# Kernel optimization log

Hardware: AMD Instinct MI355X
Metric: run time of the kernel (lower is better)

Reference implementation:

```python
import jax, jax.numpy as jnp
import numpy as np

EPS = 1e-5  # BatchNorm eps (torch default)

def _bn(x, gamma, beta):
    # training-mode BatchNorm over the edge/node (leading) axis, biased var
    mean = x.mean(axis=0, keepdims=True)
    var = x.var(axis=0, keepdims=True)
    return (x - mean) * jax.lax.rsqrt(var + EPS) * gamma + beta

def _silu(x):
    return x * jax.nn.sigmoid(x)

def setup_inputs() -> dict:
    N, E, H, NH = 50000, 800000, 128, 4
    HD = H // NH
    key = jax.random.key(0)
    ks = jax.random.split(key, 8)
    x = jax.random.normal(ks[0], (N, H), dtype=jnp.float32)
    weight = jax.random.uniform(ks[1], (N, 1), dtype=jnp.float32)  # positive fraction weights
    src = jax.random.randint(ks[2], (E,), 0, N)
    dst = jax.random.randint(ks[3], (E,), 0, N)
    # f: Linear(2H, 1) + BN(1)
    Wf = jax.random.normal(ks[4], (2 * H, 1), dtype=jnp.float32) * 0.05
    bf = jnp.zeros((1,), jnp.float32)
    f_gamma = jnp.ones((1,), jnp.float32)
    f_beta = jnp.zeros((1,), jnp.float32)
    # g: NH heads of Linear(2H, HD) + BN(HD), stacked on leading head axis
    Wg = jax.random.normal(ks[5], (NH, 2 * H, HD), dtype=jnp.float32) * 0.05
    bg = jnp.zeros((NH, HD), jnp.float32)
    g_gamma = jnp.ones((NH, HD), jnp.float32)
    g_beta = jnp.zeros((NH, HD), jnp.float32)
    # bn_nodes: BN(H)
    n_gamma = jnp.ones((H,), jnp.float32)
    n_beta = jnp.zeros((H,), jnp.float32)
    return dict(x=x, weight=weight, src=src, dst=dst, Wf=Wf, bf=bf,
                f_gamma=f_gamma, f_beta=f_beta, Wg=Wg, bg=bg,
                g_gamma=g_gamma, g_beta=g_beta, n_gamma=n_gamma, n_beta=n_beta)

def reference(x, weight, src, dst, Wf, bf, f_gamma, f_beta, Wg, bg, g_gamma, g_beta, n_gamma, n_beta):
    N = x.shape[0]
    E = src.shape[0]
    # per-edge concat of src/dst node features: [E, 2H]
    hihj = jnp.concatenate([x[src], x[dst]], axis=-1)
    # attention logit f(hihj) = SiLU(BN(Linear)) then exp: [E, 1]
    exp_e = jnp.exp(_silu(_bn(hihj @ Wf + bf, f_gamma, f_beta)))
    # weighted softmax-like normalization over incoming edges of each dst node
    we = weight[src] * exp_e                                   # [E, 1]
    sum_w_exp = jax.ops.segment_sum(we, dst, num_segments=N)   # [N, 1]
    a = we / sum_w_exp[dst]                                    # [E, 1]
    # multi-head message: a_ij * SiLU(BN(Linear_h(hihj))) per head, concat
    z = jnp.einsum('ed,hdk->ehk', hihj, Wg) + bg               # [E, NH, HD]
    z = _silu(_bn(z, g_gamma, g_beta))
    msg = (a[:, :, None] * z).reshape(E, -1)                   # [E, H]
    h = jax.ops.segment_sum(msg, dst, num_segments=N)          # [N, H]
    out = _bn(h, n_gamma, n_beta) + x                          # residual
    return out
```

## Files before the change

kernel.cpp:

```cpp
#include <hip/hip_runtime.h>
#include <hip/hip_bf16.h>
#include <math.h>

#define HDIM 128
#define PAD 64
typedef unsigned short ushort_t;
typedef unsigned int uint_t;
typedef __attribute__((ext_vector_type(8))) short bf16x8;
typedef __attribute__((ext_vector_type(4))) float f32x4;
typedef __attribute__((ext_vector_type(2))) float v2f;

__device__ __forceinline__ float wave_allreduce(float v){
  #pragma unroll
  for (int o = 1; o < 64; o <<= 1) v += __shfl_xor(v, o);
  return v;
}

__device__ __forceinline__ ushort_t f2bf(float f){
  uint_t u = __float_as_uint(f);
  uint_t r = (u + 0x7fffu + ((u >> 16) & 1u)) >> 16;
  return (ushort_t)r;
}

__device__ __forceinline__ v2f bf2(uint_t u){
  v2f r;
  r.x = __uint_as_float(u << 16);
  r.y = __uint_as_float(u & 0xffff0000u);
  return r;
}

__global__ __launch_bounds__(128) void k_wpack(const float* __restrict__ Wg,
    const float* __restrict__ Wf, ushort_t* __restrict__ W2t,
    int* __restrict__ cnt, int N){
  int b = blockIdx.x;
  int k = threadIdx.x;
  if (b < 272){
    float val;
    if (b < 128)       val = Wg[(size_t)(b >> 5) * 8192 + k * 32 + (b & 31)];
    else if (b < 256){ int c2 = b - 128;
                       val = Wg[(size_t)(c2 >> 5) * 8192 + (k + 128) * 32 + (c2 & 31)]; }
    else if (b == 256) val = Wf[k];
    else if (b == 257) val = Wf[128 + k];
    else               val = 0.f;
    W2t[(size_t)b * 128 + k] = f2bf(val);
  } else {
    int i = (b - 272) * 128 + k;
    if (i < N) cnt[i] = 0;
  }
}

__global__ __launch_bounds__(256) void k_gemmfill(const float* __restrict__ x,
    const ushort_t* __restrict__ W2t, const float* __restrict__ weight,
    ushort_t* __restrict__ Pb, ushort_t* __restrict__ Qb,
    float* __restrict__ v, float2* __restrict__ uw2,
    const int* __restrict__ src, const int* __restrict__ dst,
    int* __restrict__ cnt, int* __restrict__ es,
    int N, int E, int GB){
  if ((int)blockIdx.x < GB){
    int wid = __builtin_amdgcn_readfirstlane(threadIdx.x >> 6);
    int lane = threadIdx.x & 63;
    int quad = lane >> 4, col = lane & 15;
    int strip = blockIdx.x * 2 + (wid >> 1);
    int half = wid & 1;
    int n_base = strip * 16;
    if (n_base >= N) return;
    int tbeg = half * 8;
    int ntile = half ? 9 : 8;
    f32x4 acc[9];
    #pragma unroll
    for (int t = 0; t < 9; ++t) acc[t] = (f32x4){0.f, 0.f, 0.f, 0.f};
    int row = n_base + col;
    int rowc = row < N ? row : N - 1;
    const float* xr = x + (size_t)rowc * HDIM + quad * 8;
    #pragma unroll
    for (int kk = 0; kk < 4; ++kk){
      float4 a0 = *(const float4*)(xr + kk * 32);
      float4 a1 = *(const float4*)(xr + kk * 32 + 4);
      bf16x8 af;
      af[0] = (short)f2bf(a0.x); af[1] = (short)f2bf(a0.y);
      af[2] = (short)f2bf(a0.z); af[3] = (short)f2bf(a0.w);
      af[4] = (short)f2bf(a1.x); af[5] = (short)f2bf(a1.y);
      af[6] = (short)f2bf(a1.z); af[7] = (short)f2bf(a1.w);
      const ushort_t* wb = W2t + (size_t)(tbeg * 16) * 128 + (size_t)col * 128 + kk * 32 + quad * 8;
      #pragma unroll
      for (int t = 0; t < 9; ++t){
        if (t < ntile){
          bf16x8 bfr = *(const bf16x8*)(wb + (size_t)t * 16 * 128);
          acc[t] = __builtin_amdgcn_mfma_f32_16x16x32_bf16(af, bfr, acc[t], 0, 0, 0);
        }
      }
    }
    #pragma unroll
    for (int t = 0; t < 8; ++t){
      int ct = tbeg + t;
      int c = ct * 16 + col;
      #pragma unroll
      for (int r = 0; r < 4; ++r){
        int n = n_base + quad * 4 + r;
        if (n < N){
          ushort_t valb = f2bf(acc[t][r]);
          if (c < 128) Pb[(size_t)n * HDIM + c] = valb;
          else         Qb[(size_t)n * HDIM + (c - 128)] = valb;
        }
      }
    }
    if (half){
      #pragma unroll
      for (int r = 0; r < 4; ++r){
        int n = n_base + quad * 4 + r;
        if (n < N){
          float val = acc[8][r];
          if (col == 0)      uw2[n] = make_float2(val, weight[n]);
          else if (col == 1) v[n] = val;
        }
      }
    }
  } else {
    int bi = blockIdx.x - GB;
    int part = bi & 7;
    int nch = (gridDim.x - GB) >> 3;
    int chunk = bi >> 3;
    int Npp = (N + 7) >> 3;
    int lo = part * Npp;
    int hi = lo + Npp; if (hi > N) hi = N;
    int stride = nch * 256;
    int e = chunk * 256 + threadIdx.x;
#define FILL1(d, s) if ((d) >= lo && (d) < hi){ \
      int c = atomicAdd(&cnt[d], 1); \
      if (c < PAD) es[(size_t)(d) * PAD + c] = (s); }
    for (; e + 7 * stride < E; e += 8 * stride){
      int d0 = dst[e],            d1 = dst[e + stride];
      int d2 = dst[e + 2*stride], d3 = dst[e + 3*stride];
      int d4 = dst[e + 4*stride], d5 = dst[e + 5*stride];
      int d6 = dst[e + 6*stride], d7 = dst[e + 7*stride];
      int s0 = src[e],            s1 = src[e + stride];
      int s2 = src[e + 2*stride], s3 = src[e + 3*stride];
      int s4 = src[e + 4*stride], s5 = src[e + 5*stride];
      int s6 = src[e + 6*stride], s7 = src[e + 7*stride];
      FILL1(d0, s0) FILL1(d1, s1) FILL1(d2, s2) FILL1(d3, s3)
      FILL1(d4, s4) FILL1(d5, s5) FILL1(d6, s6) FILL1(d7, s7)
    }
    for (; e < E; e += stride){
      int d = dst[e];
      FILL1(d, src[e])
    }
#undef FILL1
  }
}

__global__ __launch_bounds__(256) void k_gstats(const ushort_t* __restrict__ Pb,
    const ushort_t* __restrict__ Qb, const float* __restrict__ v,
    const float2* __restrict__ uw2, const int* __restrict__ es,
    const int* __restrict__ cnt, float* __restrict__ pstatG, int N, int GB){
  int lane = threadIdx.x & 63;
  int wid = __builtin_amdgcn_readfirstlane(threadIdx.x >> 6);
  int part = ((int)blockIdx.x - GB) & 7;
  int Npp = (N + 7) >> 3;
  int lo = part * Npp;
  int hi = lo + Npp; if (hi > N) hi = N;
  int step = (gridDim.x >> 3) << 2;
  const uint_t* Pu = (const uint_t*)Pb;
  const uint_t* Qu = (const uint_t*)Qb;
  v2f gs = {0.f, 0.f}, gq = {0.f, 0.f};
  float fs = 0.f, fq = 0.f;
  int n = lo + ((blockIdx.x >> 3) << 2) + wid;
  int dnA = 0, sjA = 0; uint_t qA = 0; float vA = 0.f;
  if (n < hi){
    dnA = cnt[n];
    sjA = es[(size_t)n * PAD + lane];
    qA  = Qu[(size_t)n * 64 + lane];
    vA  = v[n];
  }
  while (n < hi){
    int nn = n + step;
    int dnB = 0, sjB = 0; uint_t qB = 0; float vB = 0.f;
    if (nn < hi){
      dnB = cnt[nn];
      sjB = es[(size_t)nn * PAD + lane];
      qB  = Qu[(size_t)nn * 64 + lane];
      vB  = v[nn];
    }
    int dn = dnA < PAD ? dnA : PAD;
    int sj = sjA;
    if (lane < dn){
      float2 uw = uw2[sj];
      float t = uw.x + vA;
      fs += t; fq = fmaf(t, t, fq);
    }
    v2f q = bf2(qA);
    int j = 0;
#define GSTAT(p) { v2f y = bf2(p) + q; gs += y; \
                   gq.x = fmaf(y.x, y.x, gq.x); gq.y = fmaf(y.y, y.y, gq.y); }
    for (; j + 7 < dn; j += 8){
      int s0=__shfl(sj,j),   s1=__shfl(sj,j+1), s2=__shfl(sj,j+2), s3=__shfl(sj,j+3);
      int s4=__shfl(sj,j+4), s5=__shfl(sj,j+5), s6=__shfl(sj,j+6), s7=__shfl(sj,j+7);
      uint_t p0=Pu[(size_t)s0*64+lane], p1=Pu[(size_t)s1*64+lane];
      uint_t p2=Pu[(size_t)s2*64+lane], p3=Pu[(size_t)s3*64+lane];
      uint_t p4=Pu[(size_t)s4*64+lane], p5=Pu[(size_t)s5*64+lane];
      uint_t p6=Pu[(size_t)s6*64+lane], p7=Pu[(size_t)s7*64+lane];
      GSTAT(p0) GSTAT(p1) GSTAT(p2) GSTAT(p3)
      GSTAT(p4) GSTAT(p5) GSTAT(p6) GSTAT(p7)
    }
    for (; j + 3 < dn; j += 4){
      int s0=__shfl(sj,j), s1=__shfl(sj,j+1), s2=__shfl(sj,j+2), s3=__shfl(sj,j+3);
      uint_t p0=Pu[(size_t)s0*64+lane], p1=Pu[(size_t)s1*64+lane];
      uint_t p2=Pu[(size_t)s2*64+lane], p3=Pu[(size_t)s3*64+lane];
      GSTAT(p0) GSTAT(p1) GSTAT(p2) GSTAT(p3)
    }
    for (; j < dn; ++j){
      int s0 = __shfl(sj, j);
      uint_t p0 = Pu[(size_t)s0*64+lane];
      GSTAT(p0)
    }
#undef GSTAT
    n = nn; dnA = dnB; sjA = sjB; qA = qB; vA = vB;
  }
  fs = wave_allreduce(fs); fq = wave_allreduce(fq);
  __shared__ float red[4][258];
  red[wid][2*lane]       = gs.x; red[wid][2*lane+1]   = gs.y;
  red[wid][128+2*lane]   = gq.x; red[wid][129+2*lane] = gq.y;
  if (lane == 0){ red[wid][256] = fs; red[wid][257] = fq; }
  __syncthreads();
  for (int c = threadIdx.x; c < 258; c += 256)
    pstatG[(size_t)blockIdx.x * 258 + c] = red[0][c] + red[1][c] + red[2][c] + red[3][c];
}

__global__ __launch_bounds__(256) void k_redfin1(const float* __restrict__ pstatG,
    int NB, const float* __restrict__ g_gamma, const float* __restrict__ g_beta,
    const float* __restrict__ f_gamma, const float* __restrict__ f_beta,
    float* __restrict__ fin, long long E){
  int j = blockIdx.x;
  int c1 = (j < 128) ? j : 256;
  int c2 = (j < 128) ? 128 + j : 257;
  double s1 = 0, s2 = 0;
  for (int b = threadIdx.x; b < NB; b += 256){
    const float* pb = pstatG + (size_t)b * 258;
    s1 += (double)pb[c1]; s2 += (double)pb[c2];
  }
  __shared__ double m1[256], m2[256];
  m1[threadIdx.x] = s1; m2[threadIdx.x] = s2;
  __syncthreads();
  for (int o = 128; o; o >>= 1){
    if (threadIdx.x < o){ m1[threadIdx.x] += m1[threadIdx.x + o];
                          m2[threadIdx.x] += m2[threadIdx.x + o]; }
    __syncthreads();
  }
  if (threadIdx.x == 0){
    double m = m1[0] / (double)E;
    double var = m2[0] / (double)E - m * m;
    if (j < 128){
      float sc = (float)((double)g_gamma[j] / sqrt(var + 1e-5));
      fin[2 + j] = sc; fin[130 + j] = g_beta[j] - (float)m * sc;
    } else {
      float sc = (float)((double)f_gamma[0] / sqrt(var + 1e-5));
      fin[0] = sc; fin[1] = f_beta[0] - (float)m * sc;
    }
  }
}

__global__ __launch_bounds__(256) void k_msg(const ushort_t* __restrict__ Pb,
    const ushort_t* __restrict__ Qb, const float* __restrict__ v,
    const float2* __restrict__ uw2, const int* __restrict__ es,
    const int* __restrict__ cnt, const float* __restrict__ fin,
    float* __restrict__ h, float* __restrict__ pstatH, int N, int GB){
  int lane = threadIdx.x & 63;
  int wid = __builtin_amdgcn_readfirstlane(threadIdx.x >> 6);
  int part = ((int)blockIdx.x - GB) & 7;
  int Npp = (N + 7) >> 3;
  int lo = part * Npp;
  int hi = lo + Npp; if (hi > N) hi = N;
  int step = (gridDim.x >> 3) << 2;
  const uint_t* Pu = (const uint_t*)Pb;
  const uint_t* Qu = (const uint_t*)Qb;
  float fsc = fin[0], fsh = fin[1];
  v2f gsc = {fin[2 + 2*lane], fin[3 + 2*lane]};
  v2f gsh = {fin[130 + 2*lane], fin[131 + 2*lane]};
  v2f hs = {0.f, 0.f}, hq = {0.f, 0.f};
  int n = lo + ((blockIdx.x >> 3) << 2) + wid;
  int dnA = 0, sjA = 0; uint_t qA = 0; float vA = 0.f;
  if (n < hi){
    dnA = cnt[n];
    sjA = es[(size_t)n * PAD + lane];
    qA  = Qu[(size_t)n * 64 + lane];
    vA  = v[n];
  }
  while (n < hi){
    int nn = n + step;
    int dnB = 0, sjB = 0; uint_t qB = 0; float vB = 0.f;
    if (nn < hi){
      dnB = cnt[nn];
      sjB = es[(size_t)nn * PAD + lane];
      qB  = Qu[(size_t)nn * 64 + lane];
      vB  = v[nn];
    }
    int dn = dnA < PAD ? dnA : PAD;
    int sj = sjA;
    float wj = 0.f;
    if (lane < dn){
      float2 uw = uw2[sj];
      float tt = fmaf(uw.x + vA, fsc, fsh);
      float sl = tt * __builtin_amdgcn_rcpf(1.f + __expf(-tt));
      wj = uw.y * __expf(sl);
    }
    v2f q = bf2(qA);
    v2f acc = {0.f, 0.f};
    int j = 0;
#define EDGE(p,a) { v2f y = (bf2(p) + q) * gsc + gsh; \
      float e0 = __expf(-y.x), e1 = __expf(-y.y); \
      float d0 = 1.f + e0, d1 = 1.f + e1; \
      float r = __builtin_amdgcn_rcpf(d0 * d1) * a; \
      acc.x = fmaf(y.x * d1, r, acc.x); acc.y = fmaf(y.y * d0, r, acc.y); }
    for (; j + 7 < dn; j += 8){
      int s0=__shfl(sj,j),   s1=__shfl(sj,j+1), s2=__shfl(sj,j+2), s3=__shfl(sj,j+3);
      int s4=__shfl(sj,j+4), s5=__shfl(sj,j+5), s6=__shfl(sj,j+6), s7=__shfl(sj,j+7);
      float a0=__shfl(wj,j),   a1=__shfl(wj,j+1), a2=__shfl(wj,j+2), a3=__shfl(wj,j+3);
      float a4=__shfl(wj,j+4), a5=__shfl(wj,j+5), a6=__shfl(wj,j+6), a7=__shfl(wj,j+7);
      uint_t p0=Pu[(size_t)s0*64+lane], p1=Pu[(size_t)s1*64+lane];
      uint_t p2=Pu[(size_t)s2*64+lane], p3=Pu[(size_t)s3*64+lane];
      uint_t p4=Pu[(size_t)s4*64+lane], p5=Pu[(size_t)s5*64+lane];
      uint_t p6=Pu[(size_t)s6*64+lane], p7=Pu[(size_t)s7*64+lane];
      EDGE(p0,a0) EDGE(p1,a1) EDGE(p2,a2) EDGE(p3,a3)
      EDGE(p4,a4) EDGE(p5,a5) EDGE(p6,a6) EDGE(p7,a7)
    }
    for (; j + 3 < dn; j += 4){
      int s0=__shfl(sj,j), s1=__shfl(sj,j+1), s2=__shfl(sj,j+2), s3=__shfl(sj,j+3);
      float a0=__shfl(wj,j), a1=__shfl(wj,j+1), a2=__shfl(wj,j+2), a3=__shfl(wj,j+3);
      uint_t p0=Pu[(size_t)s0*64+lane], p1=Pu[(size_t)s1*64+lane];
      uint_t p2=Pu[(size_t)s2*64+lane], p3=Pu[(size_t)s3*64+lane];
      EDGE(p0,a0) EDGE(p1,a1) EDGE(p2,a2) EDGE(p3,a3)
    }
    for (; j < dn; ++j){
      int s0 = __shfl(sj, j);
      float a0 = __shfl(wj, j);
      uint_t p0 = Pu[(size_t)s0*64+lane];
      EDGE(p0,a0)
    }
#undef EDGE
    float sw = wave_allreduce(wj);
    float rs = (dn > 0) ? (1.f / sw) : 0.f;
    acc.x *= rs; acc.y *= rs;
    *(float2*)&h[(size_t)n * 128 + 2*lane] = make_float2(acc.x, acc.y);
    hs += acc; hq += acc * acc;
    n = nn; dnA = dnB; sjA = sjB; qA = qB; vA = vB;
  }
  __shared__ float red[4][256];
  red[wid][2*lane]       = hs.x; red[wid][2*lane+1]   = hs.y;
  red[wid][128+2*lane]   = hq.x; red[wid][129+2*lane] = hq.y;
  __syncthreads();
  int c = threadIdx.x;
  pstatH[(size_t)blockIdx.x * 256 + c] = red[0][c] + red[1][c] + red[2][c] + red[3][c];
}

__global__ __launch_bounds__(256) void k_redfin2(const float* __restrict__ pstatH,
    int NB, const float* __restrict__ n_gamma, const float* __restrict__ n_beta,
    float* __restrict__ fin, int N){
  int j = blockIdx.x;
  double s1 = 0, s2 = 0;
  for (int b = threadIdx.x; b < NB; b += 256){
    const float* pb = pstatH + (size_t)b * 256;
    s1 += (double)pb[j]; s2 += (double)pb[128 + j];
  }
  __shared__ double m1[256], m2[256];
  m1[threadIdx.x] = s1; m2[threadIdx.x] = s2;
  __syncthreads();
  for (int o = 128; o; o >>= 1){
    if (threadIdx.x < o){ m1[threadIdx.x] += m1[threadIdx.x + o];
                          m2[threadIdx.x] += m2[threadIdx.x + o]; }
    __syncthreads();
  }
  if (threadIdx.x == 0){
    double m = m1[0] / (double)N;
    double var = m2[0] / (double)N - m * m;
    float sc = (float)((double)n_gamma[j] / sqrt(var + 1e-5));
    fin[258 + j] = sc; fin[386 + j] = n_beta[j] - (float)m * sc;
  }
}

__global__ __launch_bounds__(256) void k_out(const float* __restrict__ h,
    const float* __restrict__ x, const float* __restrict__ fin,
    float* __restrict__ out, int total4){
  int i = blockIdx.x * 256 + threadIdx.x;
  if (i >= total4) return;
  const float4* h4 = (const float4*)h; const float4* x4 = (const float4*)x;
  float4 hv = h4[i], xv = x4[i];
  int c = (i * 4) & 127;
  float4 o;
  o.x = fmaf(hv.x, fin[258 + c],     fin[386 + c])     + xv.x;
  o.y = fmaf(hv.y, fin[258 + c + 1], fin[386 + c + 1]) + xv.y;
  o.z = fmaf(hv.z, fin[258 + c + 2], fin[386 + c + 2]) + xv.z;
  o.w = fmaf(hv.w, fin[258 + c + 3], fin[386 + c + 3]) + xv.w;
  ((float4*)out)[i] = o;
}

extern "C" void kernel_launch(void* const* d_in, const int* in_sizes, int n_in,
                              void* d_out, int out_size, void* d_ws, size_t ws_size,
                              hipStream_t stream){
  const float* x       = (const float*)d_in[0];
  const float* weight  = (const float*)d_in[1];
  const int*   src     = (const int*)d_in[2];
  const int*   dst     = (const int*)d_in[3];
  const float* Wf      = (const float*)d_in[4];
  const float* f_gamma = (const float*)d_in[6];
  const float* f_beta  = (const float*)d_in[7];
  const float* Wg      = (const float*)d_in[8];
  const float* g_gamma = (const float*)d_in[10];
  const float* g_beta  = (const float*)d_in[11];
  const float* n_gamma = (const float*)d_in[12];
  const float* n_beta  = (const float*)d_in[13];
  float* out = (float*)d_out;

  int N = in_sizes[0] / HDIM;
  int E = in_sizes[2];

  char* ws = (char*)d_ws;
  size_t off = 0;
  auto alloc = [&](size_t bytes)->char*{
    char* p = ws + off; off = (off + bytes + 255) & ~(size_t)255; return p;
  };
  ushort_t* Pb    = (ushort_t*)alloc((size_t)N * HDIM * 2);
  ushort_t* Qb    = (ushort_t*)alloc((size_t)N * HDIM * 2);
  float* h        = (float*)alloc((size_t)N * HDIM * 4);
  float* v        = (float*)alloc((size_t)N * 4);
  float2* uw2     = (float2*)alloc((size_t)N * 8);
  int* es         = (int*)alloc((size_t)N * PAD * 4);
  ushort_t* W2t   = (ushort_t*)alloc((size_t)272 * 128 * 2);
  int* cnt        = (int*)alloc((size_t)N * 4);
  const int NWB = 2048;
  const int NB  = NWB;
  float*  pstatG = (float*)alloc((size_t)NB * 258 * 4);
  float*  pstatH = (float*)alloc((size_t)NB * 256 * 4);
  float*  fin    = (float*)alloc(514 * 4);

  int GB = (N + 31) / 32;
  const int FB = 1024;

  k_wpack   <<<272 + (N + 127) / 128, 128, 0, stream>>>(Wg, Wf, W2t, cnt, N);
  k_gemmfill<<<GB + FB, 256, 0, stream>>>(x, W2t, weight, Pb, Qb, v, uw2,
                                          src, dst, cnt, es, N, E, GB);
  k_gstats  <<<NWB, 256, 0, stream>>>(Pb, Qb, v, uw2, es, cnt, pstatG, N, GB);
  k_redfin1 <<<129, 256, 0, stream>>>(pstatG, NB, g_gamma, g_beta, f_gamma, f_beta, fin, (long long)E);
  k_msg     <<<NWB, 256, 0, stream>>>(Pb, Qb, v, uw2, es, cnt, fin, h, pstatH, N, GB);
  k_redfin2 <<<128, 256, 0, stream>>>(pstatH, NB, n_gamma, n_beta, fin, N);
  k_out     <<<(N * HDIM / 4 + 255) / 256, 256, 0, stream>>>(h, x, fin, out, N * HDIM / 4);
}
```

Baseline: 272.9 us.

## Split fused gemm/fill kernel and pad per-node atomic counters to avoid contention

Splits the combined GEMM+edge-bucketing kernel into separate k_fill and k_gemm launches, doubles fill blocks, and zeroes counters with hipMemsetAsync. Per-node counters are strided by 16 ints (64 bytes) so atomics on neighbouring nodes hit different cache lines, reducing false sharing. The cost is a larger, sparser counter array (more memset traffic and scattered reads in the stats and message kernels), and the fill and GEMM work no longer overlap within one launch.

```diff
diff --git a/kernel.cpp b/kernel.cpp
--- a/kernel.cpp
+++ b/kernel.cpp
@@ -4,6 +4,7 @@
 
 #define HDIM 128
 #define PAD 64
+#define CSTR 16
 typedef unsigned short ushort_t;
 typedef unsigned int uint_t;
 typedef __attribute__((ext_vector_type(8))) short bf16x8;
@@ -30,131 +31,123 @@
 }
 
 __global__ __launch_bounds__(128) void k_wpack(const float* __restrict__ Wg,
-    const float* __restrict__ Wf, ushort_t* __restrict__ W2t,
-    int* __restrict__ cnt, int N){
+    const float* __restrict__ Wf, ushort_t* __restrict__ W2t){
   int b = blockIdx.x;
   int k = threadIdx.x;
-  if (b < 272){
-    float val;
-    if (b < 128)       val = Wg[(size_t)(b >> 5) * 8192 + k * 32 + (b & 31)];
-    else if (b < 256){ int c2 = b - 128;
-                       val = Wg[(size_t)(c2 >> 5) * 8192 + (k + 128) * 32 + (c2 & 31)]; }
-    else if (b == 256) val = Wf[k];
-    else if (b == 257) val = Wf[128 + k];
-    else               val = 0.f;
-    W2t[(size_t)b * 128 + k] = f2bf(val);
-  } else {
-    int i = (b - 272) * 128 + k;
-    if (i < N) cnt[i] = 0;
-  }
-}
-
-__global__ __launch_bounds__(256) void k_gemmfill(const float* __restrict__ x,
+  float val;
+  if (b < 128)       val = Wg[(size_t)(b >> 5) * 8192 + k * 32 + (b & 31)];
+  else if (b < 256){ int c2 = b - 128;
+                     val = Wg[(size_t)(c2 >> 5) * 8192 + (k + 128) * 32 + (c2 & 31)]; }
+  else if (b == 256) val = Wf[k];
+  else if (b == 257) val = Wf[128 + k];
+  else               val = 0.f;
+  W2t[(size_t)b * 128 + k] = f2bf(val);
+}
+
+__global__ __launch_bounds__(256) void k_gemm(const float* __restrict__ x,
     const ushort_t* __restrict__ W2t, const float* __restrict__ weight,
     ushort_t* __restrict__ Pb, ushort_t* __restrict__ Qb,
-    float* __restrict__ v, float2* __restrict__ uw2,
+    float* __restrict__ v, float2* __restrict__ uw2, int N){
+  int wid = __builtin_amdgcn_readfirstlane(threadIdx.x >> 6);
+  int lane = threadIdx.x & 63;
+  int quad = lane >> 4, col = lane & 15;
+  int strip = blockIdx.x * 2 + (wid >> 1);
+  int half = wid & 1;
+  int n_base = strip * 16;
+  if (n_base >= N) return;
+  int tbeg = half * 8;
+  int ntile = half ? 9 : 8;
+  f32x4 acc[9];
+  #pragma unroll
+  for (int t = 0; t < 9; ++t) acc[t] = (f32x4){0.f, 0.f, 0.f, 0.f};
+  int row = n_base + col;
+  int rowc = row < N ? row : N - 1;
+  const float* xr = x + (size_t)rowc * HDIM + quad * 8;
+  #pragma unroll
+  for (int kk = 0; kk < 4; ++kk){
+    float4 a0 = *(const float4*)(xr + kk * 32);
+    float4 a1 = *(const float4*)(xr + kk * 32 + 4);
+    bf16x8 af;
+    af[0] = (short)f2bf(a0.x); af[1] = (short)f2bf(a0.y);
+    af[2] = (short)f2bf(a0.z); af[3] = (short)f2bf(a0.w);
+    af[4] = (short)f2bf(a1.x); af[5] = (short)f2bf(a1.y);
+    af[6] = (short)f2bf(a1.z); af[7] = (short)f2bf(a1.w);
+    const ushort_t* wb = W2t + (size_t)(tbeg * 16) * 128 + (size_t)col * 128 + kk * 32 + quad * 8;
+    #pragma unroll
+    for (int t = 0; t < 9; ++t){
+      if (t < ntile){
+        bf16x8 bfr = *(const bf16x8*)(wb + (size_t)t * 16 * 128);
+        acc[t] = __builtin_amdgcn_mfma_f32_16x16x32_bf16(af, bfr, acc[t], 0, 0, 0);
+      }
+    }
+  }
+  #pragma unroll
+  for (int t = 0; t < 8; ++t){
+    int ct = tbeg + t;
+    int c = ct * 16 + col;
+    #pragma unroll
+    for (int r = 0; r < 4; ++r){
+      int n = n_base + quad * 4 + r;
+      if (n < N){
+        ushort_t valb = f2bf(acc[t][r]);
+        if (c < 128) Pb[(size_t)n * HDIM + c] = valb;
+        else         Qb[(size_t)n * HDIM + (c - 128)] = valb;
+      }
+    }
+  }
+  if (half){
+    #pragma unroll
+    for (int r = 0; r < 4; ++r){
+      int n = n_base + quad * 4 + r;
+      if (n < N){
+        float val = acc[8][r];
+        if (col == 0)      uw2[n] = make_float2(val, weight[n]);
+        else if (col == 1) v[n] = val;
+      }
+    }
+  }
+}
+
+__global__ __launch_bounds__(256) void k_fill(
     const int* __restrict__ src, const int* __restrict__ dst,
-    int* __restrict__ cnt, int* __restrict__ es,
-    int N, int E, int GB){
-  if ((int)blockIdx.x < GB){
-    int wid = __builtin_amdgcn_readfirstlane(threadIdx.x >> 6);
-    int lane = threadIdx.x & 63;
-    int quad = lane >> 4, col = lane & 15;
-    int strip = blockIdx.x * 2 + (wid >> 1);
-    int half = wid & 1;
-    int n_base = strip * 16;
-    if (n_base >= N) return;
-    int tbeg = half * 8;
-    int ntile = half ? 9 : 8;
-    f32x4 acc[9];
-    #pragma unroll
-    for (int t = 0; t < 9; ++t) acc[t] = (f32x4){0.f, 0.f, 0.f, 0.f};
-    int row = n_base + col;
-    int rowc = row < N ? row : N - 1;
-    const float* xr = x + (size_t)rowc * HDIM + quad * 8;
-    #pragma unroll
-    for (int kk = 0; kk < 4; ++kk){
-      float4 a0 = *(const float4*)(xr + kk * 32);
-      float4 a1 = *(const float4*)(xr + kk * 32 + 4);
-      bf16x8 af;
-      af[0] = (short)f2bf(a0.x); af[1] = (short)f2bf(a0.y);
-      af[2] = (short)f2bf(a0.z); af[3] = (short)f2bf(a0.w);
-      af[4] = (short)f2bf(a1.x); af[5] = (short)f2bf(a1.y);
-      af[6] = (short)f2bf(a1.z); af[7] = (short)f2bf(a1.w);
-      const ushort_t* wb = W2t + (size_t)(tbeg * 16) * 128 + (size_t)col * 128 + kk * 32 + quad * 8;
-      #pragma unroll
-      for (int t = 0; t < 9; ++t){
-        if (t < ntile){
-          bf16x8 bfr = *(const bf16x8*)(wb + (size_t)t * 16 * 128);
-          acc[t] = __builtin_amdgcn_mfma_f32_16x16x32_bf16(af, bfr, acc[t], 0, 0, 0);
-        }
-      }
-    }
-    #pragma unroll
-    for (int t = 0; t < 8; ++t){
-      int ct = tbeg + t;
-      int c = ct * 16 + col;
-      #pragma unroll
-      for (int r = 0; r < 4; ++r){
-        int n = n_base + quad * 4 + r;
-        if (n < N){
-          ushort_t valb = f2bf(acc[t][r]);
-          if (c < 128) Pb[(size_t)n * HDIM + c] = valb;
-          else         Qb[(size_t)n * HDIM + (c - 128)] = valb;
-        }
-      }
-    }
-    if (half){
-      #pragma unroll
-      for (int r = 0; r < 4; ++r){
-        int n = n_base + quad * 4 + r;
-        if (n < N){
-          float val = acc[8][r];
-          if (col == 0)      uw2[n] = make_float2(val, weight[n]);
-          else if (col == 1) v[n] = val;
-        }
-      }
-    }
-  } else {
-    int bi = blockIdx.x - GB;
-    int part = bi & 7;
-    int nch = (gridDim.x - GB) >> 3;
-    int chunk = bi >> 3;
-    int Npp = (N + 7) >> 3;
-    int lo = part * Npp;
-    int hi = lo + Npp; if (hi > N) hi = N;
-    int stride = nch * 256;
-    int e = chunk * 256 + threadIdx.x;
+    int* __restrict__ cnt, int* __restrict__ es, int N, int E){
+  int part = blockIdx.x & 7;
+  int nch = gridDim.x >> 3;
+  int chunk = blockIdx.x >> 3;
+  int Npp = (N + 7) >> 3;
+  int lo = part * Npp;
+  int hi = lo + Npp; if (hi > N) hi = N;
+  int stride = nch * 256;
+  int e = chunk * 256 + threadIdx.x;
 #define FILL1(d, s) if ((d) >= lo && (d) < hi){ \
-      int c = atomicAdd(&cnt[d], 1); \
-      if (c < PAD) es[(size_t)(d) * PAD + c] = (s); }
-    for (; e + 7 * stride < E; e += 8 * stride){
-      int d0 = dst[e],            d1 = dst[e + stride];
-      int d2 = dst[e + 2*stride], d3 = dst[e + 3*stride];
-      int d4 = dst[e + 4*stride], d5 = dst[e + 5*stride];
-      int d6 = dst[e + 6*stride], d7 = dst[e + 7*stride];
-      int s0 = src[e],            s1 = src[e + stride];
-      int s2 = src[e + 2*stride], s3 = src[e + 3*stride];
-      int s4 = src[e + 4*stride], s5 = src[e + 5*stride];
-      int s6 = src[e + 6*stride], s7 = src[e + 7*stride];
-      FILL1(d0, s0) FILL1(d1, s1) FILL1(d2, s2) FILL1(d3, s3)
-      FILL1(d4, s4) FILL1(d5, s5) FILL1(d6, s6) FILL1(d7, s7)
-    }
-    for (; e < E; e += stride){
-      int d = dst[e];
-      FILL1(d, src[e])
-    }
+    int c = atomicAdd(&cnt[(size_t)(d) * CSTR], 1); \
+    if (c < PAD) es[(size_t)(d) * PAD + c] = (s); }
+  for (; e + 7 * stride < E; e += 8 * stride){
+    int d0 = dst[e],            d1 = dst[e + stride];
+    int d2 = dst[e + 2*stride], d3 = dst[e + 3*stride];
+    int d4 = dst[e + 4*stride], d5 = dst[e + 5*stride];
+    int d6 = dst[e + 6*stride], d7 = dst[e + 7*stride];
+    int s0 = src[e],            s1 = src[e + stride];
+    int s2 = src[e + 2*stride], s3 = src[e + 3*stride];
+    int s4 = src[e + 4*stride], s5 = src[e + 5*stride];
+    int s6 = src[e + 6*stride], s7 = src[e + 7*stride];
+    FILL1(d0, s0) FILL1(d1, s1) FILL1(d2, s2) FILL1(d3, s3)
+    FILL1(d4, s4) FILL1(d5, s5) FILL1(d6, s6) FILL1(d7, s7)
+  }
+  for (; e < E; e += stride){
+    int d = dst[e];
+    FILL1(d, src[e])
+  }
 #undef FILL1
-  }
 }
 
 __global__ __launch_bounds__(256) void k_gstats(const ushort_t* __restrict__ Pb,
     const ushort_t* __restrict__ Qb, const float* __restrict__ v,
     const float2* __restrict__ uw2, const int* __restrict__ es,
-    const int* __restrict__ cnt, float* __restrict__ pstatG, int N, int GB){
+    const int* __restrict__ cnt, float* __restrict__ pstatG, int N){
   int lane = threadIdx.x & 63;
   int wid = __builtin_amdgcn_readfirstlane(threadIdx.x >> 6);
-  int part = ((int)blockIdx.x - GB) & 7;
+  int part = (int)blockIdx.x & 7;
   int Npp = (N + 7) >> 3;
   int lo = part * Npp;
   int hi = lo + Npp; if (hi > N) hi = N;
@@ -166,7 +159,7 @@
   int n = lo + ((blockIdx.x >> 3) << 2) + wid;
   int dnA = 0, sjA = 0; uint_t qA = 0; float vA = 0.f;
   if (n < hi){
-    dnA = cnt[n];
+    dnA = cnt[(size_t)n * CSTR];
     sjA = es[(size_t)n * PAD + lane];
     qA  = Qu[(size_t)n * 64 + lane];
     vA  = v[n];
@@ -175,7 +168,7 @@
     int nn = n + step;
     int dnB = 0, sjB = 0; uint_t qB = 0; float vB = 0.f;
     if (nn < hi){
-      dnB = cnt[nn];
+      dnB = cnt[(size_t)nn * CSTR];
       sjB = es[(size_t)nn * PAD + lane];
       qB  = Qu[(size_t)nn * 64 + lane];
       vB  = v[nn];
@@ -262,10 +255,10 @@
     const ushort_t* __restrict__ Qb, const float* __restrict__ v,
     const float2* __restrict__ uw2, const int* __restrict__ es,
     const int* __restrict__ cnt, const float* __restrict__ fin,
-    float* __restrict__ h, float* __restrict__ pstatH, int N, int GB){
+    float* __restrict__ h, float* __restrict__ pstatH, int N){
   int lane = threadIdx.x & 63;
   int wid = __builtin_amdgcn_readfirstlane(threadIdx.x >> 6);
-  int part = ((int)blockIdx.x - GB) & 7;
+  int part = (int)blockIdx.x & 7;
   int Npp = (N + 7) >> 3;
   int lo = part * Npp;
   int hi = lo + Npp; if (hi > N) hi = N;
@@ -279,7 +272,7 @@
   int n = lo + ((blockIdx.x >> 3) << 2) + wid;
   int dnA = 0, sjA = 0; uint_t qA = 0; float vA = 0.f;
   if (n < hi){
-    dnA = cnt[n];
+    dnA = cnt[(size_t)n * CSTR];
     sjA = es[(size_t)n * PAD + lane];
     qA  = Qu[(size_t)n * 64 + lane];
     vA  = v[n];
@@ -288,7 +281,7 @@
     int nn = n + step;
     int dnB = 0, sjB = 0; uint_t qB = 0; float vB = 0.f;
     if (nn < hi){
-      dnB = cnt[nn];
+      dnB = cnt[(size_t)nn * CSTR];
       sjB = es[(size_t)nn * PAD + lane];
       qB  = Qu[(size_t)nn * 64 + lane];
       vB  = v[nn];
@@ -424,7 +417,7 @@
   float2* uw2     = (float2*)alloc((size_t)N * 8);
   int* es         = (int*)alloc((size_t)N * PAD * 4);
   ushort_t* W2t   = (ushort_t*)alloc((size_t)272 * 128 * 2);
-  int* cnt        = (int*)alloc((size_t)N * 4);
+  int* cnt        = (int*)alloc((size_t)N * CSTR * 4);
   const int NWB = 2048;
   const int NB  = NWB;
   float*  pstatG = (float*)alloc((size_t)NB * 258 * 4);
@@ -432,14 +425,15 @@
   float*  fin    = (float*)alloc(514 * 4);
 
   int GB = (N + 31) / 32;
-  const int FB = 1024;
-
-  k_wpack   <<<272 + (N + 127) / 128, 128, 0, stream>>>(Wg, Wf, W2t, cnt, N);
-  k_gemmfill<<<GB + FB, 256, 0, stream>>>(x, W2t, weight, Pb, Qb, v, uw2,
-                                          src, dst, cnt, es, N, E, GB);
-  k_gstats  <<<NWB, 256, 0, stream>>>(Pb, Qb, v, uw2, es, cnt, pstatG, N, GB);
+  const int FB = 2048;
+
+  hipMemsetAsync(cnt, 0, (size_t)N * CSTR * 4, stream);
+  k_wpack   <<<272, 128, 0, stream>>>(Wg, Wf, W2t);
+  k_fill    <<<FB, 256, 0, stream>>>(src, dst, cnt, es, N, E);
+  k_gemm    <<<GB, 256, 0, stream>>>(x, W2t, weight, Pb, Qb, v, uw2, N);
+  k_gstats  <<<NWB, 256, 0, stream>>>(Pb, Qb, v, uw2, es, cnt, pstatG, N);
   k_redfin1 <<<129, 256, 0, stream>>>(pstatG, NB, g_gamma, g_beta, f_gamma, f_beta, fin, (long long)E);
-  k_msg     <<<NWB, 256, 0, stream>>>(Pb, Qb, v, uw2, es, cnt, fin, h, pstatH, N, GB);
+  k_msg     <<<NWB, 256, 0, stream>>>(Pb, Qb, v, uw2, es, cnt, fin, h, pstatH, N);
   k_redfin2 <<<128, 256, 0, stream>>>(pstatH, NB, n_gamma, n_beta, fin, N);
   k_out     <<<(N * HDIM / 4 + 255) / 256, 256, 0, stream>>>(h, x, fin, out, N * HDIM / 4);
 }
```

Result: slower. 283.4 us (+3.9%).

## Process two dst nodes per wave with interleaved gathers and padded counters

Applied to the files above, without the earlier changes.

Each wave in the stats and message kernels now handles two destination nodes at once. Their neighbour gathers are interleaved so more independent loads are in flight, and prefetch reaches two nodes ahead. The stats kernel also factors the per-node q term out of the inner loop, accumulating sums of p and expanding (p+q)^2 algebraically afterwards. Per-node atomic counters are spaced out to one per 64 bytes to cut atomic contention in the fill, at the cost of a larger counter array to zero and more registers per wave.

```diff
diff --git a/kernel.cpp b/kernel.cpp
--- a/kernel.cpp
+++ b/kernel.cpp
@@ -4,6 +4,7 @@
 
 #define HDIM 128
 #define PAD 64
+#define CSTR 16
 typedef unsigned short ushort_t;
 typedef unsigned int uint_t;
 typedef __attribute__((ext_vector_type(8))) short bf16x8;
@@ -31,7 +32,7 @@
 
 __global__ __launch_bounds__(128) void k_wpack(const float* __restrict__ Wg,
     const float* __restrict__ Wf, ushort_t* __restrict__ W2t,
-    int* __restrict__ cnt, int N){
+    int* __restrict__ cnt, int C){
   int b = blockIdx.x;
   int k = threadIdx.x;
   if (b < 272){
@@ -45,7 +46,7 @@
     W2t[(size_t)b * 128 + k] = f2bf(val);
   } else {
     int i = (b - 272) * 128 + k;
-    if (i < N) cnt[i] = 0;
+    if (i < C) cnt[i] = 0;
   }
 }
 
@@ -117,7 +118,7 @@
     }
   } else {
     int bi = blockIdx.x - GB;
-    int part = bi & 7;
+    int part = (int)blockIdx.x & 7;
     int nch = (gridDim.x - GB) >> 3;
     int chunk = bi >> 3;
     int Npp = (N + 7) >> 3;
@@ -126,8 +127,8 @@
     int stride = nch * 256;
     int e = chunk * 256 + threadIdx.x;
 #define FILL1(d, s) if ((d) >= lo && (d) < hi){ \
-      int c = atomicAdd(&cnt[d], 1); \
-      if (c < PAD) es[(size_t)(d) * PAD + c] = (s); }
+    int c = atomicAdd(&cnt[(size_t)(d) * CSTR], 1); \
+    if (c < PAD) es[(size_t)(d) * PAD + c] = (s); }
     for (; e + 7 * stride < E; e += 8 * stride){
       int d0 = dst[e],            d1 = dst[e + stride];
       int d2 = dst[e + 2*stride], d3 = dst[e + 3*stride];
@@ -148,73 +149,85 @@
   }
 }
 
+#define SH8(sjv,jj,S) \
+  int S##0=__shfl(sjv,(jj)),   S##1=__shfl(sjv,(jj)+1), S##2=__shfl(sjv,(jj)+2), S##3=__shfl(sjv,(jj)+3), \
+      S##4=__shfl(sjv,(jj)+4), S##5=__shfl(sjv,(jj)+5), S##6=__shfl(sjv,(jj)+6), S##7=__shfl(sjv,(jj)+7);
+#define LD8(S,P) \
+  uint_t P##0=Pu[(size_t)S##0*64+lane], P##1=Pu[(size_t)S##1*64+lane], \
+         P##2=Pu[(size_t)S##2*64+lane], P##3=Pu[(size_t)S##3*64+lane], \
+         P##4=Pu[(size_t)S##4*64+lane], P##5=Pu[(size_t)S##5*64+lane], \
+         P##6=Pu[(size_t)S##6*64+lane], P##7=Pu[(size_t)S##7*64+lane];
+#define SH4(sjv,jj,S) \
+  int S##0=__shfl(sjv,(jj)),   S##1=__shfl(sjv,(jj)+1), S##2=__shfl(sjv,(jj)+2), S##3=__shfl(sjv,(jj)+3);
+#define LD4(S,P) \
+  uint_t P##0=Pu[(size_t)S##0*64+lane], P##1=Pu[(size_t)S##1*64+lane], \
+         P##2=Pu[(size_t)S##2*64+lane], P##3=Pu[(size_t)S##3*64+lane];
+
 __global__ __launch_bounds__(256) void k_gstats(const ushort_t* __restrict__ Pb,
     const ushort_t* __restrict__ Qb, const float* __restrict__ v,
     const float2* __restrict__ uw2, const int* __restrict__ es,
-    const int* __restrict__ cnt, float* __restrict__ pstatG, int N, int GB){
+    const int* __restrict__ cnt, float* __restrict__ pstatG, int N){
   int lane = threadIdx.x & 63;
   int wid = __builtin_amdgcn_readfirstlane(threadIdx.x >> 6);
-  int part = ((int)blockIdx.x - GB) & 7;
+  int part = (int)blockIdx.x & 7;
   int Npp = (N + 7) >> 3;
   int lo = part * Npp;
   int hi = lo + Npp; if (hi > N) hi = N;
-  int step = (gridDim.x >> 3) << 2;
+  int stp = (gridDim.x >> 3) << 2;
   const uint_t* Pu = (const uint_t*)Pb;
   const uint_t* Qu = (const uint_t*)Qb;
-  v2f gs = {0.f, 0.f}, gq = {0.f, 0.f};
+  v2f gs = {0.f,0.f}, gq = {0.f,0.f};
   float fs = 0.f, fq = 0.f;
-  int n = lo + ((blockIdx.x >> 3) << 2) + wid;
-  int dnA = 0, sjA = 0; uint_t qA = 0; float vA = 0.f;
-  if (n < hi){
-    dnA = cnt[n];
-    sjA = es[(size_t)n * PAD + lane];
-    qA  = Qu[(size_t)n * 64 + lane];
-    vA  = v[n];
-  }
-  while (n < hi){
-    int nn = n + step;
-    int dnB = 0, sjB = 0; uint_t qB = 0; float vB = 0.f;
-    if (nn < hi){
-      dnB = cnt[nn];
-      sjB = es[(size_t)nn * PAD + lane];
-      qB  = Qu[(size_t)nn * 64 + lane];
-      vB  = v[nn];
-    }
-    int dn = dnA < PAD ? dnA : PAD;
-    int sj = sjA;
-    if (lane < dn){
-      float2 uw = uw2[sj];
-      float t = uw.x + vA;
-      fs += t; fq = fmaf(t, t, fq);
-    }
-    v2f q = bf2(qA);
-    int j = 0;
-#define GSTAT(p) { v2f y = bf2(p) + q; gs += y; \
-                   gq.x = fmaf(y.x, y.x, gq.x); gq.y = fmaf(y.y, y.y, gq.y); }
-    for (; j + 7 < dn; j += 8){
-      int s0=__shfl(sj,j),   s1=__shfl(sj,j+1), s2=__shfl(sj,j+2), s3=__shfl(sj,j+3);
-      int s4=__shfl(sj,j+4), s5=__shfl(sj,j+5), s6=__shfl(sj,j+6), s7=__shfl(sj,j+7);
-      uint_t p0=Pu[(size_t)s0*64+lane], p1=Pu[(size_t)s1*64+lane];
-      uint_t p2=Pu[(size_t)s2*64+lane], p3=Pu[(size_t)s3*64+lane];
-      uint_t p4=Pu[(size_t)s4*64+lane], p5=Pu[(size_t)s5*64+lane];
-      uint_t p6=Pu[(size_t)s6*64+lane], p7=Pu[(size_t)s7*64+lane];
-      GSTAT(p0) GSTAT(p1) GSTAT(p2) GSTAT(p3)
-      GSTAT(p4) GSTAT(p5) GSTAT(p6) GSTAT(p7)
-    }
-    for (; j + 3 < dn; j += 4){
-      int s0=__shfl(sj,j), s1=__shfl(sj,j+1), s2=__shfl(sj,j+2), s3=__shfl(sj,j+3);
-      uint_t p0=Pu[(size_t)s0*64+lane], p1=Pu[(size_t)s1*64+lane];
-      uint_t p2=Pu[(size_t)s2*64+lane], p3=Pu[(size_t)s3*64+lane];
-      GSTAT(p0) GSTAT(p1) GSTAT(p2) GSTAT(p3)
-    }
-    for (; j < dn; ++j){
-      int s0 = __shfl(sj, j);
-      uint_t p0 = Pu[(size_t)s0*64+lane];
-      GSTAT(p0)
-    }
-#undef GSTAT
-    n = nn; dnA = dnB; sjA = sjB; qA = qB; vA = vB;
-  }
+  int n0 = lo + ((blockIdx.x >> 3) << 2) + wid;
+  int n1 = n0 + stp;
+  int dnA=0,sjA=0; uint_t qAu=0; float vA=0.f;
+  int dnB=0,sjB=0; uint_t qBu=0; float vB=0.f;
+  if (n0 < hi){ dnA=cnt[(size_t)n0*CSTR]; sjA=es[(size_t)n0*PAD+lane];
+                qAu=Qu[(size_t)n0*64+lane]; vA=v[n0]; }
+  if (n1 < hi){ dnB=cnt[(size_t)n1*CSTR]; sjB=es[(size_t)n1*PAD+lane];
+                qBu=Qu[(size_t)n1*64+lane]; vB=v[n1]; }
+#define GST(p,Sv,Qv) { v2f y=bf2(p); Sv+=y; Qv.x=fmaf(y.x,y.x,Qv.x); Qv.y=fmaf(y.y,y.y,Qv.y); }
+#define GED8(P,Sv,Qv) GST(P##0,Sv,Qv) GST(P##1,Sv,Qv) GST(P##2,Sv,Qv) GST(P##3,Sv,Qv) \
+                      GST(P##4,Sv,Qv) GST(P##5,Sv,Qv) GST(P##6,Sv,Qv) GST(P##7,Sv,Qv)
+#define GED4(P,Sv,Qv) GST(P##0,Sv,Qv) GST(P##1,Sv,Qv) GST(P##2,Sv,Qv) GST(P##3,Sv,Qv)
+  while (n0 < hi){
+    int m0 = n0 + 2*stp, m1 = n1 + 2*stp;
+    int dnC=0,sjC=0; uint_t qCu=0; float vC=0.f;
+    int dnD=0,sjD=0; uint_t qDu=0; float vD=0.f;
+    if (m0 < hi){ dnC=cnt[(size_t)m0*CSTR]; sjC=es[(size_t)m0*PAD+lane];
+                  qCu=Qu[(size_t)m0*64+lane]; vC=v[m0]; }
+    if (m1 < hi){ dnD=cnt[(size_t)m1*CSTR]; sjD=es[(size_t)m1*PAD+lane];
+                  qDu=Qu[(size_t)m1*64+lane]; vD=v[m1]; }
+    int dA = dnA < PAD ? dnA : PAD;
+    int dB = (n1 < hi) ? (dnB < PAD ? dnB : PAD) : 0;
+    if (lane < dA){ float2 uw = uw2[sjA]; float t = uw.x + vA; fs += t; fq = fmaf(t,t,fq); }
+    if (lane < dB){ float2 uw = uw2[sjB]; float t = uw.x + vB; fs += t; fq = fmaf(t,t,fq); }
+    v2f qa = bf2(qAu), qb = bf2(qBu);
+    v2f SnA={0.f,0.f}, SSA={0.f,0.f}, SnB={0.f,0.f}, SSB={0.f,0.f};
+    int j0 = 0, j1 = 0;
+    for (; j0 + 7 < dA && j1 + 7 < dB; j0 += 8, j1 += 8){
+      SH8(sjA,j0,xa) SH8(sjB,j1,xb)
+      LD8(xa,pa) LD8(xb,pb)
+      GED8(pa,SnA,SSA) GED8(pb,SnB,SSB)
+    }
+    for (; j0 + 7 < dA; j0 += 8){ SH8(sjA,j0,xa) LD8(xa,pa) GED8(pa,SnA,SSA) }
+    for (; j0 + 3 < dA; j0 += 4){ SH4(sjA,j0,xa) LD4(xa,pa) GED4(pa,SnA,SSA) }
+    for (; j0 < dA; ++j0){ int s0=__shfl(sjA,j0); uint_t p0=Pu[(size_t)s0*64+lane]; GST(p0,SnA,SSA) }
+    for (; j1 + 7 < dB; j1 += 8){ SH8(sjB,j1,xb) LD8(xb,pb) GED8(pb,SnB,SSB) }
+    for (; j1 + 3 < dB; j1 += 4){ SH4(sjB,j1,xb) LD4(xb,pb) GED4(pb,SnB,SSB) }
+    for (; j1 < dB; ++j1){ int s0=__shfl(sjB,j1); uint_t p0=Pu[(size_t)s0*64+lane]; GST(p0,SnB,SSB) }
+    float dAf = (float)dA, dBf = (float)dB;
+    gs.x += SnA.x + SnB.x + dAf*qa.x + dBf*qb.x;
+    gs.y += SnA.y + SnB.y + dAf*qa.y + dBf*qb.y;
+    gq.x += SSA.x + SSB.x + qa.x*fmaf(dAf,qa.x,2.f*SnA.x) + qb.x*fmaf(dBf,qb.x,2.f*SnB.x);
+    gq.y += SSA.y + SSB.y + qa.y*fmaf(dAf,qa.y,2.f*SnA.y) + qb.y*fmaf(dBf,qb.y,2.f*SnB.y);
+    n0 = m0; n1 = m1;
+    dnA=dnC; sjA=sjC; qAu=qCu; vA=vC;
+    dnB=dnD; sjB=sjD; qBu=qDu; vB=vD;
+  }
+#undef GST
+#undef GED8
+#undef GED4
   fs = wave_allreduce(fs); fq = wave_allreduce(fq);
   __shared__ float red[4][258];
   red[wid][2*lane]       = gs.x; red[wid][2*lane+1]   = gs.y;
@@ -262,87 +275,99 @@
     const ushort_t* __restrict__ Qb, const float* __restrict__ v,
     const float2* __restrict__ uw2, const int* __restrict__ es,
     const int* __restrict__ cnt, const float* __restrict__ fin,
-    float* __restrict__ h, float* __restrict__ pstatH, int N, int GB){
+    float* __restrict__ h, float* __restrict__ pstatH, int N){
   int lane = threadIdx.x & 63;
   int wid = __builtin_amdgcn_readfirstlane(threadIdx.x >> 6);
-  int part = ((int)blockIdx.x - GB) & 7;
+  int part = (int)blockIdx.x & 7;
   int Npp = (N + 7) >> 3;
   int lo = part * Npp;
   int hi = lo + Npp; if (hi > N) hi = N;
-  int step = (gridDim.x >> 3) << 2;
+  int stp = (gridDim.x >> 3) << 2;
   const uint_t* Pu = (const uint_t*)Pb;
   const uint_t* Qu = (const uint_t*)Qb;
   float fsc = fin[0], fsh = fin[1];
   v2f gsc = {fin[2 + 2*lane], fin[3 + 2*lane]};
   v2f gsh = {fin[130 + 2*lane], fin[131 + 2*lane]};
-  v2f hs = {0.f, 0.f}, hq = {0.f, 0.f};
-  int n = lo + ((blockIdx.x >> 3) << 2) + wid;
-  int dnA = 0, sjA = 0; uint_t qA = 0; float vA = 0.f;
-  if (n < hi){
-    dnA = cnt[n];
-    sjA = es[(size_t)n * PAD + lane];
-    qA  = Qu[(size_t)n * 64 + lane];
-    vA  = v[n];
-  }
-  while (n < hi){
-    int nn = n + step;
-    int dnB = 0, sjB = 0; uint_t qB = 0; float vB = 0.f;
-    if (nn < hi){
-      dnB = cnt[nn];
-      sjB = es[(size_t)nn * PAD + lane];
-      qB  = Qu[(size_t)nn * 64 + lane];
-      vB  = v[nn];
-    }
-    int dn = dnA < PAD ? dnA : PAD;
-    int sj = sjA;
-    float wj = 0.f;
-    if (lane < dn){
-      float2 uw = uw2[sj];
+  v2f hs = {0.f,0.f}, hq = {0.f,0.f};
+  int n0 = lo + ((blockIdx.x >> 3) << 2) + wid;
+  int n1 = n0 + stp;
+  int dnA=0,sjA=0; uint_t qAu=0; float vA=0.f;
+  int dnB=0,sjB=0; uint_t qBu=0; float vB=0.f;
+  if (n0 < hi){ dnA=cnt[(size_t)n0*CSTR]; sjA=es[(size_t)n0*PAD+lane];
+                qAu=Qu[(size_t)n0*64+lane]; vA=v[n0]; }
+  if (n1 < hi){ dnB=cnt[(size_t)n1*CSTR]; sjB=es[(size_t)n1*PAD+lane];
+                qBu=Qu[(size_t)n1*64+lane]; vB=v[n1]; }
+#define EDGE(p,a,qv,av) { v2f y = (bf2(p) + qv) * gsc + gsh; \
+      float e0 = __expf(-y.x), e1 = __expf(-y.y); \
+      float d0 = 1.f + e0, d1 = 1.f + e1; \
+      float r = __builtin_amdgcn_rcpf(d0 * d1) * (a); \
+      av.x = fmaf(y.x * d1, r, av.x); av.y = fmaf(y.y * d0, r, av.y); }
+#define ASH8(wjv,jj,A) \
+  float A##0=__shfl(wjv,(jj)),   A##1=__shfl(wjv,(jj)+1), A##2=__shfl(wjv,(jj)+2), A##3=__shfl(wjv,(jj)+3), \
+        A##4=__shfl(wjv,(jj)+4), A##5=__shfl(wjv,(jj)+5), A##6=__shfl(wjv,(jj)+6), A##7=__shfl(wjv,(jj)+7);
+#define ASH4(wjv,jj,A) \
+  float A##0=__shfl(wjv,(jj)),   A##1=__shfl(wjv,(jj)+1), A##2=__shfl(wjv,(jj)+2), A##3=__shfl(wjv,(jj)+3);
+#define MED8(P,A,qv,av) EDGE(P##0,A##0,qv,av) EDGE(P##1,A##1,qv,av) EDGE(P##2,A##2,qv,av) EDGE(P##3,A##3,qv,av) \
+                        EDGE(P##4,A##4,qv,av) EDGE(P##5,A##5,qv,av) EDGE(P##6,A##6,qv,av) EDGE(P##7,A##7,qv,av)
+#define MED4(P,A,qv,av) EDGE(P##0,A##0,qv,av) EDGE(P##1,A##1,qv,av) EDGE(P##2,A##2,qv,av) EDGE(P##3,A##3,qv,av)
+  while (n0 < hi){
+    int m0 = n0 + 2*stp, m1 = n1 + 2*stp;
+    int dnC=0,sjC=0; uint_t qCu=0; float vC=0.f;
+    int dnD=0,sjD=0; uint_t qDu=0; float vD=0.f;
+    if (m0 < hi){ dnC=cnt[(size_t)m0*CSTR]; sjC=es[(size_t)m0*PAD+lane];
+                  qCu=Qu[(size_t)m0*64+lane]; vC=v[m0]; }
+    if (m1 < hi){ dnD=cnt[(size_t)m1*CSTR]; sjD=es[(size_t)m1*PAD+lane];
+                  qDu=Qu[(size_t)m1*64+lane]; vD=v[m1]; }
+    int dA = dnA < PAD ? dnA : PAD;
+    int dB = (n1 < hi) ? (dnB < PAD ? dnB : PAD) : 0;
+    float wjA = 0.f, wjB = 0.f;
+    if (lane < dA){ float2 uw = uw2[sjA];
       float tt = fmaf(uw.x + vA, fsc, fsh);
       float sl = tt * __builtin_amdgcn_rcpf(1.f + __expf(-tt));
-      wj = uw.y * __expf(sl);
-    }
-    v2f q = bf2(qA);
-    v2f acc = {0.f, 0.f};
-    int j = 0;
-#define EDGE(p,a) { v2f y = (bf2(p) + q) * gsc + gsh; \
-      float e0 = __expf(-y.x), e1 = __expf(-y.y); \
-      float d0 = 1.f + e0, d1 = 1.f + e1; \
-      float r = __builtin_amdgcn_rcpf(d0 * d1) * a; \
-      acc.x = fmaf(y.x * d1, r, acc.x); acc.y = fmaf(y.y * d0, r, acc.y); }
-    for (; j + 7 < dn; j += 8){
-      int s0=__shfl(sj,j),   s1=__shfl(sj,j+1), s2=__shfl(sj,j+2), s3=__shfl(sj,j+3);
-      int s4=__shfl(sj,j+4), s5=__shfl(sj,j+5), s6=__shfl(sj,j+6), s7=__shfl(sj,j+7);
-      float a0=__shfl(wj,j),   a1=__shfl(wj,j+1), a2=__shfl(wj,j+2), a3=__shfl(wj,j+3);
-      float a4=__shfl(wj,j+4), a5=__shfl(wj,j+5), a6=__shfl(wj,j+6), a7=__shfl(wj,j+7);
-      uint_t p0=Pu[(size_t)s0*64+lane], p1=Pu[(size_t)s1*64+lane];
-      uint_t p2=Pu[(size_t)s2*64+lane], p3=Pu[(size_t)s3*64+lane];
-      uint_t p4=Pu[(size_t)s4*64+lane], p5=Pu[(size_t)s5*64+lane];
-      uint_t p6=Pu[(size_t)s6*64+lane], p7=Pu[(size_t)s7*64+lane];
-      EDGE(p0,a0) EDGE(p1,a1) EDGE(p2,a2) EDGE(p3,a3)
-      EDGE(p4,a4) EDGE(p5,a5) EDGE(p6,a6) EDGE(p7,a7)
-    }
-    for (; j + 3 < dn; j += 4){
-      int s0=__shfl(sj,j), s1=__shfl(sj,j+1), s2=__shfl(sj,j+2), s3=__shfl(sj,j+3);
-      float a0=__shfl(wj,j), a1=__shfl(wj,j+1), a2=__shfl(wj,j+2), a3=__shfl(wj,j+3);
-      uint_t p0=Pu[(size_t)s0*64+lane], p1=Pu[(size_t)s1*64+lane];
-      uint_t p2=Pu[(size_t)s2*64+lane], p3=Pu[(size_t)s3*64+lane];
-      EDGE(p0,a0) EDGE(p1,a1) EDGE(p2,a2) EDGE(p3,a3)
-    }
-    for (; j < dn; ++j){
-      int s0 = __shfl(sj, j);
-      float a0 = __shfl(wj, j);
-      uint_t p0 = Pu[(size_t)s0*64+lane];
-      EDGE(p0,a0)
-    }
+      wjA = uw.y * __expf(sl); }
+    if (lane < dB){ float2 uw = uw2[sjB];
+      float tt = fmaf(uw.x + vB, fsc, fsh);
+      float sl = tt * __builtin_amdgcn_rcpf(1.f + __expf(-tt));
+      wjB = uw.y * __expf(sl); }
+    v2f qa = bf2(qAu), qb = bf2(qBu);
+    v2f accA = {0.f,0.f}, accB = {0.f,0.f};
+    int j0 = 0, j1 = 0;
+    for (; j0 + 7 < dA && j1 + 7 < dB; j0 += 8, j1 += 8){
+      SH8(sjA,j0,xa) SH8(sjB,j1,xb)
+      ASH8(wjA,j0,aa) ASH8(wjB,j1,ab)
+      LD8(xa,pa) LD8(xb,pb)
+      MED8(pa,aa,qa,accA) MED8(pb,ab,qb,accB)
+    }
+    for (; j0 + 7 < dA; j0 += 8){ SH8(sjA,j0,xa) ASH8(wjA,j0,aa) LD8(xa,pa) MED8(pa,aa,qa,accA) }
+    for (; j0 + 3 < dA; j0 += 4){ SH4(sjA,j0,xa) ASH4(wjA,j0,aa) LD4(xa,pa) MED4(pa,aa,qa,accA) }
+    for (; j0 < dA; ++j0){ int s0=__shfl(sjA,j0); float a0=__shfl(wjA,j0);
+                           uint_t p0=Pu[(size_t)s0*64+lane]; EDGE(p0,a0,qa,accA) }
+    for (; j1 + 7 < dB; j1 += 8){ SH8(sjB,j1,xb) ASH8(wjB,j1,ab) LD8(xb,pb) MED8(pb,ab,qb,accB) }
+    for (; j1 + 3 < dB; j1 += 4){ SH4(sjB,j1,xb) ASH4(wjB,j1,ab) LD4(xb,pb) MED4(pb,ab,qb,accB) }
+    for (; j1 < dB; ++j1){ int s0=__shfl(sjB,j1); float a0=__shfl(wjB,j1);
+                           uint_t p0=Pu[(size_t)s0*64+lane]; EDGE(p0,a0,qb,accB) }
+    float swA = wjA, swB = wjB;
+    #pragma unroll
+    for (int o = 1; o < 64; o <<= 1){ swA += __shfl_xor(swA, o); swB += __shfl_xor(swB, o); }
+    float rsA = (dA > 0) ? (1.f / swA) : 0.f;
+    float rsB = (dB > 0) ? (1.f / swB) : 0.f;
+    accA.x *= rsA; accA.y *= rsA;
+    accB.x *= rsB; accB.y *= rsB;
+    *(float2*)&h[(size_t)n0 * 128 + 2*lane] = make_float2(accA.x, accA.y);
+    hs += accA; hq += accA * accA;
+    if (n1 < hi){
+      *(float2*)&h[(size_t)n1 * 128 + 2*lane] = make_float2(accB.x, accB.y);
+      hs += accB; hq += accB * accB;
+    }
+    n0 = m0; n1 = m1;
+    dnA=dnC; sjA=sjC; qAu=qCu; vA=vC;
+    dnB=dnD; sjB=sjD; qBu=qDu; vB=vD;
+  }
 #undef EDGE
-    float sw = wave_allreduce(wj);
-    float rs = (dn > 0) ? (1.f / sw) : 0.f;
-    acc.x *= rs; acc.y *= rs;
-    *(float2*)&h[(size_t)n * 128 + 2*lane] = make_float2(acc.x, acc.y);
-    hs += acc; hq += acc * acc;
-    n = nn; dnA = dnB; sjA = sjB; qA = qB; vA = vB;
-  }
+#undef ASH8
+#undef ASH4
+#undef MED8
+#undef MED4
   __shared__ float red[4][256];
   red[wid][2*lane]       = hs.x; red[wid][2*lane+1]   = hs.y;
   red[wid][128+2*lane]   = hq.x; red[wid][129+2*lane] = hq.y;
@@ -424,7 +449,7 @@
   float2* uw2     = (float2*)alloc((size_t)N * 8);
   int* es         = (int*)alloc((size_t)N * PAD * 4);
   ushort_t* W2t   = (ushort_t*)alloc((size_t)272 * 128 * 2);
-  int* cnt        = (int*)alloc((size_t)N * 4);
+  int* cnt        = (int*)alloc((size_t)N * CSTR * 4);
   const int NWB = 2048;
   const int NB  = NWB;
   float*  pstatG = (float*)alloc((size_t)NB * 258 * 4);
@@ -433,13 +458,14 @@
 
   int GB = (N + 31) / 32;
   const int FB = 1024;
-
-  k_wpack   <<<272 + (N + 127) / 128, 128, 0, stream>>>(Wg, Wf, W2t, cnt, N);
+  int CT = N * CSTR;
+
+  k_wpack   <<<272 + (CT + 127) / 128, 128, 0, stream>>>(Wg, Wf, W2t, cnt, CT);
   k_gemmfill<<<GB + FB, 256, 0, stream>>>(x, W2t, weight, Pb, Qb, v, uw2,
                                           src, dst, cnt, es, N, E, GB);
-  k_gstats  <<<NWB, 256, 0, stream>>>(Pb, Qb, v, uw2, es, cnt, pstatG, N, GB);
+  k_gstats  <<<NWB, 256, 0, stream>>>(Pb, Qb, v, uw2, es, cnt, pstatG, N);
   k_redfin1 <<<129, 256, 0, stream>>>(pstatG, NB, g_gamma, g_beta, f_gamma, f_beta, fin, (long long)E);
-  k_msg     <<<NWB, 256, 0, stream>>>(Pb, Qb, v, uw2, es, cnt, fin, h, pstatH, N, GB);
+  k_msg     <<<NWB, 256, 0, stream>>>(Pb, Qb, v, uw2, es, cnt, fin, h, pstatH, N);
   k_redfin2 <<<128, 256, 0, stream>>>(pstatH, NB, n_gamma, n_beta, fin, N);
   k_out     <<<(N * HDIM / 4 + 255) / 256, 256, 0, stream>>>(h, x, fin, out, N * HDIM / 4);
 }
```

After: 280.2 us. 2.7% more time.
